# Kernel optimization log

Measured on AMD Instinct MI355X. Metric: run time of the kernel, lower is better.

Reference implementation:

```python
import jax, jax.numpy as jnp
import numpy as np

NEG = -1000000000.0  # mask fill value used by the TF code
LEAKY_ALPHA = 0.2
TEMPERATURE = 0.5
TOP_K = 32
SHARPEN_POWER = 2.0
UNITS = 64
HEADS = 4
IN_DIM = 128
B, N = 8, 512


def sparsemax(logits):
    # Faithful port of the TF sparsemax with masked-entry handling.
    valid = (logits > -100000000.0).astype(logits.dtype)
    n_valid = jnp.maximum(jnp.sum(valid, axis=-1, keepdims=True), 1.0)
    masked = jnp.where(valid > 0, logits, 0.0)
    valid_mean = jnp.sum(masked, axis=-1, keepdims=True) / n_valid
    z = logits - valid_mean
    z = jnp.where(valid > 0, z, NEG)
    z_sorted = -jnp.sort(-z, axis=-1)  # descending
    dim = z.shape[-1]
    range_k = jnp.arange(1, dim + 1, dtype=z.dtype)
    cumsum = jnp.cumsum(z_sorted, axis=-1)
    threshold = (cumsum - 1.0) / range_k
    support = (z_sorted > threshold).astype(z.dtype)
    k_star = jnp.maximum(jnp.sum(support, axis=-1, keepdims=True), 1.0)
    tau = (jnp.sum(z_sorted * support, axis=-1, keepdims=True) - 1.0) / k_star
    return jnp.maximum(z - tau, 0.0) * valid


def setup_inputs() -> dict:
    key = jax.random.key(0)
    k1, k2, k3, k4, k5 = jax.random.split(key, 5)
    features = jax.random.normal(k1, (B, N, IN_DIM), dtype=jnp.float32)
    adjacency = jax.random.randint(k2, (B, N, N), 0, 2, dtype=jnp.int32)
    # glorot-ish scaled params
    s_w = np.sqrt(6.0 / (IN_DIM + UNITS)).astype(np.float32)
    s_a = np.sqrt(6.0 / (UNITS + 1)).astype(np.float32)
    W_src = jax.random.uniform(k3, (HEADS, IN_DIM, UNITS), jnp.float32, -s_w, s_w)
    W_dst = jax.random.uniform(k4, (HEADS, IN_DIM, UNITS), jnp.float32, -s_w, s_w)
    a = jax.random.uniform(k5, (HEADS, UNITS, 1), jnp.float32, -s_a, s_a)
    return {"features": features, "adjacency": adjacency, "W_src": W_src, "W_dst": W_dst, "a": a}


def reference(features, adjacency, W_src, W_dst, a):
    adj_f = adjacency.astype(jnp.float32)
    eye = jnp.eye(N, dtype=jnp.float32)[None]  # self loops
    mask = ((adj_f + eye) > 0)
    head_outs = []
    for h in range(HEADS):
        h_src = features @ W_src[h]          # [B,N,U]
        h_dst = features @ W_dst[h]          # [B,N,U]
        pairwise = h_src[:, :, None, :] + h_dst[:, None, :, :]   # [B,N,N,U]
        pairwise = jnp.where(pairwise > 0, pairwise, LEAKY_ALPHA * pairwise)
        scores = jnp.einsum('biju,u->bij', pairwise, a[h, :, 0])  # [B,N,N]
        scores = scores / jnp.sqrt(jnp.float32(UNITS))            # scale_scores=True
        scores = jnp.where(mask, scores, NEG)
        top_vals, _ = jax.lax.top_k(scores, TOP_K)
        kth = top_vals[:, :, -1:]
        scores = jnp.where(scores >= kth, scores, NEG)
        scores = scores / TEMPERATURE
        attn = sparsemax(scores)
        attn = jnp.power(attn + 1e-09, SHARPEN_POWER)
        attn = attn / (jnp.sum(attn, axis=-1, keepdims=True) + 1e-09)
        head_outs.append(attn @ h_src)       # [B,N,U]
    return jnp.mean(jnp.stack(head_outs, axis=-1), axis=-1)
```

## Files before the change

kernel.cpp:

```cpp
#include <hip/hip_runtime.h>
#include <hip/hip_bf16.h>

#define HEADS 4
#define UNITS 64
#define IN_DIM_ 128
#define NN 512
#define TOPK 32
#define NEGV -1e9f

__device__ __forceinline__ float readlane_f(float v, int l) {
    return __int_as_float(__builtin_amdgcn_readlane(__float_as_int(v), l));
}
__device__ __forceinline__ unsigned mapu(float x) {
    unsigned b = __float_as_uint(x);
    return b ^ ((unsigned)((int)b >> 31) | 0x80000000u);
}
__device__ __forceinline__ int mbcnt64(unsigned long long m) {
    return __builtin_amdgcn_mbcnt_hi((unsigned)(m >> 32),
           __builtin_amdgcn_mbcnt_lo((unsigned)(m & 0xFFFFFFFFull), 0u));
}

__global__ __launch_bounds__(256) void gat_k1(
    const float* __restrict__ feat, const float* __restrict__ Wsrc,
    const float* __restrict__ Wdst, const float* __restrict__ a,
    float* __restrict__ hsrc, float* __restrict__ hdstT,
    float* __restrict__ As, float* __restrict__ Ad)
{
    const int bx = blockIdx.x;
    const int rb = bx & 127;
    const int h  = (bx >> 7) & 3;
    const int sd = bx >> 9;
    const int r0 = rb * 32;
    const float* W = (sd ? Wdst : Wsrc) + h * (IN_DIM_ * UNITS);

    __shared__ float xs[32][132];
    __shared__ float wsh[128][64];
    __shared__ float ot[32][65];

    const int tid = threadIdx.x;
    #pragma unroll
    for (int it = 0; it < 4; ++it) {
        int f4 = it * 256 + tid;
        int r = f4 >> 5, c4 = (f4 & 31) << 2;
        *(float4*)&xs[r][c4] = *(const float4*)&feat[(r0 + r) * IN_DIM_ + c4];
    }
    #pragma unroll
    for (int it = 0; it < 8; ++it) {
        int f4 = it * 256 + tid;
        int r = f4 >> 4, c4 = (f4 & 15) << 2;
        *(float4*)&wsh[r][c4] = *(const float4*)&W[r * UNITS + c4];
    }
    __syncthreads();

    const int tx = tid & 15, ty = tid >> 4;
    float acc[2][4] = {{0.f,0.f,0.f,0.f},{0.f,0.f,0.f,0.f}};
    for (int k4 = 0; k4 < 128; k4 += 4) {
        float4 x0 = *(const float4*)&xs[ty*2+0][k4];
        float4 x1 = *(const float4*)&xs[ty*2+1][k4];
        float4 w0 = *(const float4*)&wsh[k4+0][tx*4];
        float4 w1 = *(const float4*)&wsh[k4+1][tx*4];
        float4 w2 = *(const float4*)&wsh[k4+2][tx*4];
        float4 w3 = *(const float4*)&wsh[k4+3][tx*4];
#define K1STEP(xc, wq) \
        acc[0][0]=fmaf(x0.xc,wq.x,acc[0][0]); acc[0][1]=fmaf(x0.xc,wq.y,acc[0][1]); \
        acc[0][2]=fmaf(x0.xc,wq.z,acc[0][2]); acc[0][3]=fmaf(x0.xc,wq.w,acc[0][3]); \
        acc[1][0]=fmaf(x1.xc,wq.x,acc[1][0]); acc[1][1]=fmaf(x1.xc,wq.y,acc[1][1]); \
        acc[1][2]=fmaf(x1.xc,wq.z,acc[1][2]); acc[1][3]=fmaf(x1.xc,wq.w,acc[1][3]);
        K1STEP(x, w0) K1STEP(y, w1) K1STEP(z, w2) K1STEP(w, w3)
#undef K1STEP
    }
    if (sd == 0) {
        #pragma unroll
        for (int r = 0; r < 2; ++r) {
            float4 v = make_float4(acc[r][0], acc[r][1], acc[r][2], acc[r][3]);
            *(float4*)&hsrc[(h * 4096 + r0 + ty*2 + r) * UNITS + tx*4] = v;
        }
    }
    #pragma unroll
    for (int r = 0; r < 2; ++r) {
        #pragma unroll
        for (int c = 0; c < 4; ++c) ot[ty*2 + r][tx*4 + c] = acc[r][c];
    }
    __syncthreads();
    if (sd == 1) {
        const int bidx = r0 >> 9, jb0 = r0 & 511;
        #pragma unroll
        for (int it = 0; it < 8; ++it) {
            int f = it * 256 + tid;
            int u = f >> 5, jl = f & 31;
            hdstT[(((h*8 + bidx) * 64 + u) << 9) + jb0 + jl] = ot[jl][u];
        }
    }
    if (tid < 32) {
        float s = 0.f;
        for (int u = 0; u < 64; ++u) s += ot[tid][u] * a[h*64 + u];
        (sd ? Ad : As)[h * 4096 + r0 + tid] = s;
    }
}

__global__ __launch_bounds__(256, 8) void gat_k2(
    const float* __restrict__ hsrc, const float* __restrict__ hdstT,
    const float* __restrict__ As_g, const float* __restrict__ Ad_g,
    const int* __restrict__ adj, const float* __restrict__ a_g,
    float* __restrict__ out)
{
    __shared__ float zAll[4 * 72];
    __shared__ int   jAll[4 * 72];

    const int tid = threadIdx.x;
    const int w = tid >> 6, lane = tid & 63;
    float* zbuf = zAll + w * 72;
    int*   jbuf = jAll + w * 72;

    const int bid = blockIdx.x;
    const int swz = (bid & 7) * 256 + (bid >> 3);
    const int wid = swz * 4 + w;
    const int slice = wid >> 8;
    const int rp    = wid & 255;
    const int h = slice >> 3, b = slice & 7;
    const int i0 = rp * 2;
    const unsigned VALIDU = mapu(-5e7f);

    const float* dbase = hdstT + (slice << 15);

    const float aqreg = 0.05f * a_g[h*64 + lane];
    const int grow0 = b*512 + i0;
    const float sreg0 = hsrc[((h*4096 + grow0) << 6) + lane];
    const float sreg1 = hsrc[((h*4096 + grow0 + 1) << 6) + lane];
    const float Asi0 = As_g[h*4096 + grow0];
    const float Asi1 = As_g[h*4096 + grow0 + 1];

    float acc0[8] = {0,0,0,0,0,0,0,0};
    float acc1[8] = {0,0,0,0,0,0,0,0};
    #pragma unroll 8
    for (int u = 0; u < 64; ++u) {
        const float4 d0 = *(const float4*)&dbase[(u << 9) + (lane << 2)];
        const float4 d1 = *(const float4*)&dbase[(u << 9) + 256 + (lane << 2)];
        const float su0 = readlane_f(sreg0, u);
        const float su1 = readlane_f(sreg1, u);
        const float qu  = readlane_f(aqreg, u);
        acc0[0]=fmaf(qu,fabsf(su0+d0.x),acc0[0]); acc0[1]=fmaf(qu,fabsf(su0+d0.y),acc0[1]);
        acc0[2]=fmaf(qu,fabsf(su0+d0.z),acc0[2]); acc0[3]=fmaf(qu,fabsf(su0+d0.w),acc0[3]);
        acc0[4]=fmaf(qu,fabsf(su0+d1.x),acc0[4]); acc0[5]=fmaf(qu,fabsf(su0+d1.y),acc0[5]);
        acc0[6]=fmaf(qu,fabsf(su0+d1.z),acc0[6]); acc0[7]=fmaf(qu,fabsf(su0+d1.w),acc0[7]);
        acc1[0]=fmaf(qu,fabsf(su1+d0.x),acc1[0]); acc1[1]=fmaf(qu,fabsf(su1+d0.y),acc1[1]);
        acc1[2]=fmaf(qu,fabsf(su1+d0.z),acc1[2]); acc1[3]=fmaf(qu,fabsf(su1+d0.w),acc1[3]);
        acc1[4]=fmaf(qu,fabsf(su1+d1.x),acc1[4]); acc1[5]=fmaf(qu,fabsf(su1+d1.y),acc1[5]);
        acc1[6]=fmaf(qu,fabsf(su1+d1.z),acc1[6]); acc1[7]=fmaf(qu,fabsf(su1+d1.w),acc1[7]);
    }
    const float4 ad0 = *(const float4*)&Ad_g[h*4096 + b*512 + (lane << 2)];
    const float4 ad1 = *(const float4*)&Ad_g[h*4096 + b*512 + 256 + (lane << 2)];

    float outAcc[2];
    for (int rr = 0; rr < 2; ++rr) {
        const int i = i0 + rr;
        const int grow = b*512 + i;
        const float Asi = rr ? Asi1 : Asi0;
        const float* accp = rr ? acc1 : acc0;
        const int4 av0 = *(const int4*)&adj[(grow << 9) + (lane << 2)];
        const int4 av1 = *(const int4*)&adj[(grow << 9) + 256 + (lane << 2)];
        const float adv[8] = {ad0.x,ad0.y,ad0.z,ad0.w,ad1.x,ad1.y,ad1.z,ad1.w};
        const int   avv[8] = {av0.x,av0.y,av0.z,av0.w,av1.x,av1.y,av1.z,av1.w};
        float m[8]; int jj[8];
        #pragma unroll
        for (int k = 0; k < 8; ++k) {
            int j = ((k >> 2) << 8) + (lane << 2) + (k & 3);
            jj[k] = j;
            float sc = accp[k] + 0.075f * (Asi + adv[k]);
            m[k] = (avv[k] > 0 || j == i) ? sc : NEGV;
        }
        unsigned ux[8];
        #pragma unroll
        for (int k = 0; k < 8; ++k) ux[k] = mapu(m[k]);
        unsigned prefix = 0u;
        for (int bit = 31; bit >= 0; --bit) {
            unsigned T = prefix | (1u << bit);
            int c0 = 0;
            #pragma unroll
            for (int k = 0; k < 8; ++k) c0 += __popcll(__ballot(ux[k] >= T));
            if (c0 >= TOPK) {
                prefix = T;
                if (c0 == TOPK) break;
            }
        }
        int cnt = 0;
        #pragma unroll
        for (int k = 0; k < 8; ++k) {
            bool sv = (ux[k] >= prefix) && (ux[k] > VALIDU);
            unsigned long long mm = __ballot(sv);
            if (sv) {
                int pos = cnt + mbcnt64(mm);
                if (pos < 64) { zbuf[pos] = 2.f * m[k]; jbuf[pos] = jj[k]; }
            }
            cnt += __popcll(mm);
        }
        if (cnt > 64) cnt = 64;
        if (lane < 4) { zbuf[cnt + lane] = -1e30f; jbuf[cnt + lane] = 0; }
        const int nt4 = (cnt + 3) >> 2;
        float zmax = -1e30f;
        for (int t4 = 0; t4 < nt4; ++t4) {
            float4 q = *(const float4*)&zbuf[t4 << 2];
            zmax = fmaxf(zmax, fmaxf(fmaxf(q.x, q.y), fmaxf(q.z, q.w)));
        }
        float lo = zmax - 1.0f, width = 1.0f;
        for (int r3 = 0; r3 < 3; ++r3) {
            float step = width * 0.015625f;
            float tc = lo + step * (float)(lane + 1);
            float f = 0.f;
            for (int t4 = 0; t4 < nt4; ++t4) {
                float4 q = *(const float4*)&zbuf[t4 << 2];
                f += fmaxf(q.x - tc, 0.f) + fmaxf(q.y - tc, 0.f)
                   + fmaxf(q.z - tc, 0.f) + fmaxf(q.w - tc, 0.f);
            }
            int p = __popcll(__ballot(f >= 1.0f));
            lo += step * (float)p;
            width = step;
        }
        const float taum = lo + 0.5f * width;
        float S = 0.f; int ks = 0;
        for (int t4 = 0; t4 < nt4; ++t4) {
            float4 q = *(const float4*)&zbuf[t4 << 2];
            if (q.x > taum) { S += q.x; ++ks; }
            if (q.y > taum) { S += q.y; ++ks; }
            if (q.z > taum) { S += q.z; ++ks; }
            if (q.w > taum) { S += q.w; ++ks; }
        }
        if (ks == 0) { ks = 1; S = zmax; }
        const float tau = (S - 1.0f) / (float)ks;
        float pl = 0.f;
        if (lane < cnt) {
            float wv = fmaxf(zbuf[lane] - tau, 0.f) + 1e-9f;
            pl = wv * wv;
        }
        float dsum = pl;
        #pragma unroll
        for (int d = 1; d < 64; d <<= 1) dsum += __shfl_xor(dsum, d, 64);
        const float denom = dsum + 1e-9f + (float)(512 - cnt) * 1e-18f;
        const float rd = 1.0f / denom;
        float oa = 0.f;
        #pragma unroll
        for (int t = 0; t < TOPK; ++t) {
            float zt = zbuf[t];
            int jt = jbuf[t] & 511;
            float wv = fmaxf(zt - tau, 0.f) + 1e-9f;
            wv = wv * wv * rd;
            if (t >= cnt) wv = 0.f;
            oa = fmaf(wv, hsrc[((h*4096 + b*512 + jt) << 6) + lane], oa);
        }
        for (int t = TOPK; t < cnt; ++t) {
            float zt = zbuf[t];
            int jt = jbuf[t] & 511;
            float wv = fmaxf(zt - tau, 0.f) + 1e-9f;
            wv = wv * wv * rd;
            oa = fmaf(wv, hsrc[((h*4096 + b*512 + jt) << 6) + lane], oa);
        }
        outAcc[rr] = oa;
    }
    #pragma unroll
    for (int rr = 0; rr < 2; ++rr) {
        int i = i0 + rr;
        atomicAdd(&out[((b*512 + i) << 6) + lane], 0.25f * outAcc[rr]);
    }
}

extern "C" void kernel_launch(void* const* d_in, const int* in_sizes, int n_in,
                              void* d_out, int out_size, void* d_ws, size_t ws_size,
                              hipStream_t stream) {
    const float* feat = (const float*)d_in[0];
    const int*   adj  = (const int*)d_in[1];
    const float* Wsrc = (const float*)d_in[2];
    const float* Wdst = (const float*)d_in[3];
    const float* a    = (const float*)d_in[4];
    float* out = (float*)d_out;
    float* ws  = (float*)d_ws;
    float* hsrc  = ws;
    float* hdstT = ws + 1048576;
    float* As    = ws + 2097152;
    float* Ad    = ws + 2113536;

    hipMemsetAsync(d_out, 0, (size_t)out_size * sizeof(float), stream);
    gat_k1<<<1024, 256, 0, stream>>>(feat, Wsrc, Wdst, a, hsrc, hdstT, As, Ad);
    gat_k2<<<2048, 256, 0, stream>>>(hsrc, hdstT, As, Ad, adj, a, out);
}
```

Baseline: 175.7 us.

## Compute sparsemax tau by iterative support refinement and broadcast weights via readlane

The bisection search for the sparsemax threshold is replaced by an exact iterative loop. Each lane holds one candidate value, the loop computes tau from the current support with a wave reduction, and it shrinks the support until it stops changing. Per-candidate weights are computed once per lane and broadcast with readlane in the gather loop, instead of being recomputed from shared memory every step. The projection kernel also drops its shared-memory staging of W and reads the weights directly from global memory, which saves LDS and a copy but may cost more global/cache traffic.

```diff
diff --git a/kernel.cpp b/kernel.cpp
--- a/kernel.cpp
+++ b/kernel.cpp
@@ -34,7 +34,6 @@
     const float* W = (sd ? Wdst : Wsrc) + h * (IN_DIM_ * UNITS);
 
     __shared__ float xs[32][132];
-    __shared__ float wsh[128][64];
     __shared__ float ot[32][65];
 
     const int tid = threadIdx.x;
@@ -44,12 +43,6 @@
         int r = f4 >> 5, c4 = (f4 & 31) << 2;
         *(float4*)&xs[r][c4] = *(const float4*)&feat[(r0 + r) * IN_DIM_ + c4];
     }
-    #pragma unroll
-    for (int it = 0; it < 8; ++it) {
-        int f4 = it * 256 + tid;
-        int r = f4 >> 4, c4 = (f4 & 15) << 2;
-        *(float4*)&wsh[r][c4] = *(const float4*)&W[r * UNITS + c4];
-    }
     __syncthreads();
 
     const int tx = tid & 15, ty = tid >> 4;
@@ -57,10 +50,10 @@
     for (int k4 = 0; k4 < 128; k4 += 4) {
         float4 x0 = *(const float4*)&xs[ty*2+0][k4];
         float4 x1 = *(const float4*)&xs[ty*2+1][k4];
-        float4 w0 = *(const float4*)&wsh[k4+0][tx*4];
-        float4 w1 = *(const float4*)&wsh[k4+1][tx*4];
-        float4 w2 = *(const float4*)&wsh[k4+2][tx*4];
-        float4 w3 = *(const float4*)&wsh[k4+3][tx*4];
+        float4 w0 = *(const float4*)&W[(k4+0) * UNITS + tx*4];
+        float4 w1 = *(const float4*)&W[(k4+1) * UNITS + tx*4];
+        float4 w2 = *(const float4*)&W[(k4+2) * UNITS + tx*4];
+        float4 w3 = *(const float4*)&W[(k4+3) * UNITS + tx*4];
 #define K1STEP(xc, wq) \
         acc[0][0]=fmaf(x0.xc,wq.x,acc[0][0]); acc[0][1]=fmaf(x0.xc,wq.y,acc[0][1]); \
         acc[0][2]=fmaf(x0.xc,wq.z,acc[0][2]); acc[0][3]=fmaf(x0.xc,wq.w,acc[0][3]); \
@@ -196,63 +189,43 @@
         }
         if (cnt > 64) cnt = 64;
         if (lane < 4) { zbuf[cnt + lane] = -1e30f; jbuf[cnt + lane] = 0; }
-        const int nt4 = (cnt + 3) >> 2;
-        float zmax = -1e30f;
-        for (int t4 = 0; t4 < nt4; ++t4) {
-            float4 q = *(const float4*)&zbuf[t4 << 2];
-            zmax = fmaxf(zmax, fmaxf(fmaxf(q.x, q.y), fmaxf(q.z, q.w)));
-        }
-        float lo = zmax - 1.0f, width = 1.0f;
-        for (int r3 = 0; r3 < 3; ++r3) {
-            float step = width * 0.015625f;
-            float tc = lo + step * (float)(lane + 1);
-            float f = 0.f;
-            for (int t4 = 0; t4 < nt4; ++t4) {
-                float4 q = *(const float4*)&zbuf[t4 << 2];
-                f += fmaxf(q.x - tc, 0.f) + fmaxf(q.y - tc, 0.f)
-                   + fmaxf(q.z - tc, 0.f) + fmaxf(q.w - tc, 0.f);
-            }
-            int p = __popcll(__ballot(f >= 1.0f));
-            lo += step * (float)p;
-            width = step;
-        }
-        const float taum = lo + 0.5f * width;
-        float S = 0.f; int ks = 0;
-        for (int t4 = 0; t4 < nt4; ++t4) {
-            float4 q = *(const float4*)&zbuf[t4 << 2];
-            if (q.x > taum) { S += q.x; ++ks; }
-            if (q.y > taum) { S += q.y; ++ks; }
-            if (q.z > taum) { S += q.z; ++ks; }
-            if (q.w > taum) { S += q.w; ++ks; }
-        }
-        if (ks == 0) { ks = 1; S = zmax; }
-        const float tau = (S - 1.0f) / (float)ks;
-        float pl = 0.f;
-        if (lane < cnt) {
-            float wv = fmaxf(zbuf[lane] - tau, 0.f) + 1e-9f;
-            pl = wv * wv;
-        }
+        float zl = zbuf[lane];
+        int   jl = jbuf[lane] & 511;
+        bool act = (lane < cnt);
+        if (!act) { zl = 0.f; jl = 0; }
+        float tau;
+        unsigned long long am = __ballot(act);
+        bool cur = act;
+        for (;;) {
+            float s = cur ? zl : 0.f;
+            #pragma unroll
+            for (int d = 1; d < 64; d <<= 1) s += __shfl_xor(s, d, 64);
+            const int kk = __popcll(am);
+            tau = (s - 1.0f) / (float)kk;
+            bool na = cur && (zl > tau);
+            unsigned long long nm = __ballot(na);
+            if (nm == am || nm == 0ull) break;
+            am = nm; cur = na;
+        }
+        float wv = fmaxf(zl - tau, 0.f) + 1e-9f;
+        float pl = (lane < cnt) ? wv * wv : 0.f;
         float dsum = pl;
         #pragma unroll
         for (int d = 1; d < 64; d <<= 1) dsum += __shfl_xor(dsum, d, 64);
-        const float denom = dsum + 1e-9f + (float)(512 - cnt) * 1e-18f;
-        const float rd = 1.0f / denom;
+        const float rd = 1.0f / (dsum + 1e-9f + (float)(512 - cnt) * 1e-18f);
+        const float wlane = pl * rd;
+        const float* hb = hsrc + ((h*4096 + b*512) << 6) + lane;
         float oa = 0.f;
         #pragma unroll
         for (int t = 0; t < TOPK; ++t) {
-            float zt = zbuf[t];
-            int jt = jbuf[t] & 511;
-            float wv = fmaxf(zt - tau, 0.f) + 1e-9f;
-            wv = wv * wv * rd;
-            if (t >= cnt) wv = 0.f;
-            oa = fmaf(wv, hsrc[((h*4096 + b*512 + jt) << 6) + lane], oa);
+            float wt = readlane_f(wlane, t);
+            int   jt = __builtin_amdgcn_readlane(jl, t);
+            oa = fmaf(wt, hb[jt << 6], oa);
         }
         for (int t = TOPK; t < cnt; ++t) {
-            float zt = zbuf[t];
-            int jt = jbuf[t] & 511;
-            float wv = fmaxf(zt - tau, 0.f) + 1e-9f;
-            wv = wv * wv * rd;
-            oa = fmaf(wv, hsrc[((h*4096 + b*512 + jt) << 6) + lane], oa);
+            float wt = readlane_f(wlane, t);
+            int   jt = __builtin_amdgcn_readlane(jl, t);
+            oa = fmaf(wt, hb[jt << 6], oa);
         }
         outAcc[rr] = oa;
     }
```

After: 153.5 us. 12.6% less time.
